# Kernel tuning notes

Hardware: AMD Instinct MI355X
Metric: run time of the kernel (lower is better)

The kernel has to match this reference:

```python
import jax, jax.numpy as jnp
import numpy as np

TSZ, BSZ, E, H = 1024, 8, 1024, 16


def setup_inputs() -> dict:
    key = jax.random.key(0)
    ks = jax.random.split(key, 7)
    s = 0.02
    return {
        "q": jax.random.normal(ks[0], (TSZ, BSZ, E), jnp.float32),
        "k": jax.random.normal(ks[1], (TSZ, BSZ, E), jnp.float32),
        "v": jax.random.normal(ks[2], (TSZ, BSZ, E), jnp.float32),
        "in_proj_weight": jax.random.normal(ks[3], (3 * E, E), jnp.float32) * s,
        "in_proj_bias": jax.random.normal(ks[4], (3 * E,), jnp.float32) * s,
        "out_proj_weight": jax.random.normal(ks[5], (E, E), jnp.float32) * s,
        "out_proj_bias": jax.random.normal(ks[6], (E,), jnp.float32) * s,
        "num_heads": H,
    }


def reference(q, k, v, in_proj_weight, in_proj_bias, out_proj_weight, out_proj_bias, num_heads):
    tsz, bsz, embed_dim = q.shape
    head_dim = embed_dim // num_heads
    scaling = float(head_dim) ** -0.5

    # in-projections (F.linear: x @ W.T + b), weight sliced into q/k/v chunks
    qp = q @ in_proj_weight[:embed_dim].T + in_proj_bias[:embed_dim]
    kp = k @ in_proj_weight[embed_dim:2 * embed_dim].T + in_proj_bias[embed_dim:2 * embed_dim]
    vp = v @ in_proj_weight[2 * embed_dim:].T + in_proj_bias[2 * embed_dim:]
    qp = qp * scaling

    # (tsz, bsz, E) -> (bsz*H, tsz, head_dim)
    def to_heads(x):
        return x.reshape(tsz, bsz * num_heads, head_dim).transpose(1, 0, 2)

    qh, kh, vh = to_heads(qp), to_heads(kp), to_heads(vp)

    # scaled dot-product attention (no mask, dropout p=0)
    scores = jnp.einsum('bqd,bkd->bqk', qh, kh)  # [bsz*H, tsz, tsz]
    weights = jax.nn.softmax(scores, axis=-1)
    attn = jnp.einsum('bqk,bkd->bqd', weights, vh)

    # back to (tsz, bsz, E), then out projection
    attn = attn.transpose(1, 0, 2).reshape(tsz, bsz, embed_dim)
    out = attn @ out_proj_weight.T + out_proj_bias
    return out
```

## Files before the change

kernel.cpp:

```cpp
#include <hip/hip_runtime.h>

typedef __bf16 bf16;
typedef __attribute__((ext_vector_type(8))) __bf16 v8bf;
typedef __attribute__((ext_vector_type(4))) __bf16 v4bf;
typedef __attribute__((ext_vector_type(4))) float f32x4;

static_assert(sizeof(v8bf) == 16, "v8bf must be 16B");

#define MFMA16(a, b, c) __builtin_amdgcn_mfma_f32_16x16x32_bf16((a), (b), (c), 0, 0, 0)

__device__ __forceinline__ void async_lds16(const bf16* g, bf16* l) {
  __builtin_amdgcn_global_load_lds(
      (__attribute__((address_space(1))) void*)(g),
      (__attribute__((address_space(3))) void*)(l), 16, 0, 0);
}

__global__ __launch_bounds__(256) void cvt_kernel(
    const float* __restrict__ q, const float* __restrict__ k,
    const float* __restrict__ v, const float* __restrict__ wi,
    const float* __restrict__ wo, bf16* __restrict__ xq, bf16* __restrict__ xk,
    bf16* __restrict__ xv, bf16* __restrict__ Wb, bf16* __restrict__ Wob) {
  int idx = blockIdx.x * 256 + threadIdx.x;
  const float4* src;
  v4bf* dst;
  int off;
  if (idx < 2097152)      { src = (const float4*)q;  dst = (v4bf*)xq;  off = idx; }
  else if (idx < 4194304) { src = (const float4*)k;  dst = (v4bf*)xk;  off = idx - 2097152; }
  else if (idx < 6291456) { src = (const float4*)v;  dst = (v4bf*)xv;  off = idx - 4194304; }
  else if (idx < 7077888) { src = (const float4*)wi; dst = (v4bf*)Wb;  off = idx - 6291456; }
  else                    { src = (const float4*)wo; dst = (v4bf*)Wob; off = idx - 7077888; }
  float4 f = src[off];
  v4bf b;
  b[0] = (bf16)f.x; b[1] = (bf16)f.y; b[2] = (bf16)f.z; b[3] = (bf16)f.w;
  dst[off] = b;
}

#define AB2_(AB) (((AB) + 2) % 3)

#define STG_A4(AB, KO)                                                        \
  do {                                                                        \
    _Pragma("unroll") for (int cc = 0; cc < 4; ++cc)                          \
        async_lds16(Xa + (size_t)cc * 65536 + srcoff + (KO),                  \
                    Asmb + (AB) * 8192 + cc * 2048 + wdst);                   \
  } while (0)

#define STG_B2(BB, KO)                                                        \
  do {                                                                        \
    _Pragma("unroll") for (int cc = 0; cc < 2; ++cc)                          \
        async_lds16(Wbase + (size_t)cc * 65536 + srcoff + (KO),               \
                    Bsmb + (BB) * 4096 + cc * 2048 + wdst);                   \
  } while (0)

#define RD_A(AB, G)                                                           \
  _Pragma("unroll") for (int f = 0; f < 4; ++f)                               \
      ar[f] = *(const v8bf*)&Asmb[(AB) * 8192 + arow + (G) * 2048 +           \
                                  f * 512 + slot8];

#define RD_B(BB)                                                              \
  _Pragma("unroll") for (int nf = 0; nf < 4; ++nf)                            \
      br[nf] = *(const v8bf*)&Bsmb[(BB) * 4096 + brow + nf * 512 + slot8];

#define MM(OFF)                                                               \
  __builtin_amdgcn_s_setprio(1);                                              \
  _Pragma("unroll") for (int f = 0; f < 4; ++f)                               \
      _Pragma("unroll") for (int nf = 0; nf < 4; ++nf)                        \
          acc[(OFF) + f][nf] = MFMA16(ar[f], br[nf], acc[(OFF) + f][nf]);     \
  __builtin_amdgcn_s_setprio(0);

#define STEP(T, AB, BB, SB, SA, VM)                                           \
  do {                                                                        \
    v8bf ar[4], br[4];                                                        \
    RD_A(AB, 0);                                                              \
    RD_B(BB);                                                                 \
    if (SB) STG_B2((BB) ^ 1, ((T) + 1) * 32);                                 \
    __builtin_amdgcn_s_barrier();                                             \
    MM(0);                                                                    \
    RD_A(AB, 1);                                                              \
    if (SA) STG_A4(AB2_(AB), ((T) + 2) * 32);                                 \
    if ((VM) == 4) { asm volatile("s_waitcnt vmcnt(4)" ::: "memory"); }       \
    else if ((VM) == 0) { asm volatile("s_waitcnt vmcnt(0)" ::: "memory"); }  \
    __builtin_amdgcn_s_barrier();                                             \
    MM(4);                                                                    \
  } while (0)

#define GEMM_PRELUDE()                                                        \
  const int tid = threadIdx.x;                                                \
  const int w = tid >> 6, l = tid & 63, quad = l >> 4, lr = l & 15;           \
  const int wmg = w >> 1, wng = w & 1;                                        \
  const int slot8 = (quad ^ ((lr >> 1) & 3)) * 8;                             \
  const int arow = (wmg * 128 + lr) * 32;                                     \
  const int brow = (wng * 64 + lr) * 32;                                      \
  const int wdst = (tid & ~63) * 8;                                           \
  const int srow = tid >> 2;                                                  \
  const int srcoff = srow * 1024 + (((tid & 3) ^ ((srow >> 1) & 3)) * 8);     \
  f32x4 acc[8][4] = {};                                                       \
  STG_A4(0, 0);                                                               \
  STG_B2(0, 0);                                                               \
  STG_A4(1, 32);                                                              \
  asm volatile("s_waitcnt vmcnt(4)" ::: "memory");                            \
  __builtin_amdgcn_s_barrier();                                               \
  _Pragma("unroll 1") for (int tt = 0; tt < 30; tt += 6) {                    \
    STEP(tt + 0, 0, 0, 1, 1, 4);                                              \
    STEP(tt + 1, 1, 1, 1, 1, 4);                                              \
    STEP(tt + 2, 2, 0, 1, 1, 4);                                              \
    STEP(tt + 3, 0, 1, 1, 1, 4);                                              \
    STEP(tt + 4, 1, 0, 1, 1, 4);                                              \
    STEP(tt + 5, 2, 1, 1, 1, 4);                                              \
  }                                                                           \
  STEP(30, 0, 0, 1, 0, 0);                                                    \
  STEP(31, 1, 1, 0, 0, -1);

__global__ __launch_bounds__(256, 2) void qkv_proj_kernel(
    const bf16* __restrict__ xq, const bf16* __restrict__ xk,
    const bf16* __restrict__ xv, const bf16* __restrict__ Wb,
    const float* __restrict__ bias, bf16* __restrict__ oq,
    bf16* __restrict__ ok, bf16* __restrict__ ov) {
  __shared__ bf16 Asm3[3][8192];
  __shared__ bf16 Bsm3[2][4096];
  bf16* Asmb = &Asm3[0][0];
  bf16* Bsmb = &Bsm3[0][0];
  const int L = blockIdx.x;
  const int g = L >> 5;
  const int c = g >> 3;
  const int n0 = (g & 7) * 128;
  const int m0 = (L & 31) * 256;
  const bf16* X = (c == 0) ? xq : (c == 1) ? xk : xv;
  bf16* outp = (c == 0) ? oq : (c == 1) ? ok : ov;
  const bf16* Xa = X + (size_t)m0 * 1024;
  const bf16* Wbase = Wb + ((size_t)(c * 1024 + n0)) * 1024;

  GEMM_PRELUDE();

  const float scale = (c == 0) ? 0.125f : 1.0f;
#pragma unroll
  for (int mf = 0; mf < 8; ++mf)
#pragma unroll
    for (int nf = 0; nf < 4; ++nf) {
      const int n = n0 + wng * 64 + nf * 16 + lr;
      const float bn = bias[c * 1024 + n];
      const int hh = n >> 6, d = n & 63;
#pragma unroll
      for (int j = 0; j < 4; ++j) {
        const int m = m0 + wmg * 128 + (mf >> 2) * 64 + (mf & 3) * 16 +
                      quad * 4 + j;
        const int t_ = m >> 3, b = m & 7;
        outp[((size_t)((b * 16 + hh) * 1024 + t_)) * 64 + d] =
            (bf16)((acc[mf][nf][j] + bn) * scale);
      }
    }
}

__global__ __launch_bounds__(256) void transpose_v_kernel(const bf16* __restrict__ vin,
                                                          bf16* __restrict__ vout) {
  __shared__ bf16 tile[64][72];
  const int bh = blockIdx.x;
  const int t0 = blockIdx.y * 64;
  const int tid = threadIdx.x;
  const int row = tid >> 2, cg = (tid & 3) * 16;
  const bf16* src = vin + ((size_t)bh * 1024 + t0 + row) * 64 + cg;
#pragma unroll
  for (int i = 0; i < 2; ++i) {
    v8bf x = *(const v8bf*)(src + i * 8);
#pragma unroll
    for (int jj = 0; jj < 8; ++jj) tile[row][cg + i * 8 + jj] = x[jj];
  }
  __syncthreads();
  const int d = tid >> 2, tg = (tid & 3) * 16;
  bf16* dst = vout + ((size_t)bh * 64 + d) * 1024 + t0 + tg;
  v8bf o0, o1;
#pragma unroll
  for (int i = 0; i < 8; ++i) o0[i] = tile[tg + i][d];
#pragma unroll
  for (int i = 0; i < 8; ++i) o1[i] = tile[tg + 8 + i][d];
  *(v8bf*)dst = o0;
  *(v8bf*)(dst + 8) = o1;
}

#define KSTR 72
#define VSTR 136

__global__ __launch_bounds__(256, 2) void attn_kernel(const bf16* __restrict__ qh,
                                                      const bf16* __restrict__ kh,
                                                      const bf16* __restrict__ vT,
                                                      bf16* __restrict__ attn_out) {
  __shared__ bf16 Ksm[128 * KSTR];
  __shared__ bf16 Vsm[64 * VSTR];
  __shared__ bf16 Psm[128 * VSTR];
  const int L = blockIdx.x;
  const int bh = (L & 7) * 16 + ((L >> 3) & 15);
  const int t0 = (L >> 7) * 128;
  const int tid = threadIdx.x;
  const int w = tid >> 6, l = tid & 63, quad = l >> 4, lr = l & 15;
  const int qr0 = t0 + w * 32;

  const bf16* khead = kh + (size_t)bh * 1024 * 64;
  const bf16* vhead = vT + (size_t)bh * 64 * 1024;

  const size_t qbase = ((size_t)bh * 1024 + qr0 + lr) * 64 + quad * 8;
  const v8bf bq00 = *(const v8bf*)(qh + qbase);
  const v8bf bq01 = *(const v8bf*)(qh + qbase + 32);
  const v8bf bq10 = *(const v8bf*)(qh + qbase + 1024);
  const v8bf bq11 = *(const v8bf*)(qh + qbase + 1024 + 32);

  const int krow = tid >> 1, kd = (tid & 1) * 32;
  const int vrow = tid >> 2, vk = (tid & 3) * 32;
  const bf16* kg = khead + (size_t)krow * 64 + kd;
  const bf16* vg = vhead + (size_t)vrow * 1024 + vk;
  bf16* Kw = &Ksm[krow * KSTR + kd];
  bf16* Vw = &Vsm[vrow * VSTR + vk];
  bf16* Pw = &Psm[w * 32 * VSTR];

  v8bf kst[4], vst[4];
#pragma unroll
  for (int i = 0; i < 4; ++i) kst[i] = *(const v8bf*)(kg + i * 8);
#pragma unroll
  for (int i = 0; i < 4; ++i) vst[i] = *(const v8bf*)(vg + i * 8);

  float rsum0 = 0.0f, rsum1 = 0.0f;
  f32x4 oacc0[4] = {}, oacc1[4] = {};

  for (int c = 0; c < 8; ++c) {
    __syncthreads();
#pragma unroll
    for (int i = 0; i < 4; ++i) *(v8bf*)(Kw + i * 8) = kst[i];
#pragma unroll
    for (int i = 0; i < 4; ++i) *(v8bf*)(Vw + i * 8) = vst[i];
    __syncthreads();
    if (c < 7) {
      const bf16* kg2 = kg + (size_t)(c + 1) * 128 * 64;
      const bf16* vg2 = vg + (c + 1) * 128;
#pragma unroll
      for (int i = 0; i < 4; ++i) kst[i] = *(const v8bf*)(kg2 + i * 8);
#pragma unroll
      for (int i = 0; i < 4; ++i) vst[i] = *(const v8bf*)(vg2 + i * 8);
    }

#pragma unroll
    for (int kt = 0; kt < 8; ++kt) {
      const v8bf ak0 = *(const v8bf*)&Ksm[(kt * 16 + lr) * KSTR + quad * 8];
      const v8bf ak1 = *(const v8bf*)&Ksm[(kt * 16 + lr) * KSTR + 32 + quad * 8];
      f32x4 a = {};
      a = MFMA16(ak0, bq00, a);
      a = MFMA16(ak1, bq01, a);
      f32x4 b = {};
      b = MFMA16(ak0, bq10, b);
      b = MFMA16(ak1, bq11, b);
      v4bf pb0, pb1;
#pragma unroll
      for (int j = 0; j < 4; ++j) {
        const float p0 = __expf(a[j]);
        const float p1 = __expf(b[j]);
        rsum0 += p0;
        rsum1 += p1;
        pb0[j] = (bf16)p0;
        pb1[j] = (bf16)p1;
      }
      *(v4bf*)(Pw + lr * VSTR + kt * 16 + quad * 4) = pb0;
      *(v4bf*)(Pw + (16 + lr) * VSTR + kt * 16 + quad * 4) = pb1;
    }

#pragma unroll
    for (int ks = 0; ks < 4; ++ks) {
      const v8bf pa0 = *(const v8bf*)(Pw + lr * VSTR + ks * 32 + quad * 8);
      const v8bf pa1 = *(const v8bf*)(Pw + (16 + lr) * VSTR + ks * 32 + quad * 8);
#pragma unroll
      for (int dt = 0; dt < 4; ++dt) {
        const v8bf vb = *(const v8bf*)&Vsm[(dt * 16 + lr) * VSTR + ks * 32 + quad * 8];
        oacc0[dt] = MFMA16(pa0, vb, oacc0[dt]);
        oacc1[dt] = MFMA16(pa1, vb, oacc1[dt]);
      }
    }
  }

  rsum0 += __shfl_xor(rsum0, 16);
  rsum0 += __shfl_xor(rsum0, 32);
  rsum1 += __shfl_xor(rsum1, 16);
  rsum1 += __shfl_xor(rsum1, 32);
  const float inv0 = 1.0f / rsum0;
  const float inv1 = 1.0f / rsum1;
  const int b = bh >> 4, h = bh & 15;
#pragma unroll
  for (int j = 0; j < 4; ++j) {
    const float i0 = __shfl(inv0, quad * 4 + j);
    const float i1 = __shfl(inv1, quad * 4 + j);
    const int t0j = qr0 + quad * 4 + j;
#pragma unroll
    for (int dt = 0; dt < 4; ++dt) {
      attn_out[((size_t)(t0j * 8 + b)) * 1024 + h * 64 + dt * 16 + lr] =
          (bf16)(oacc0[dt][j] * i0);
      attn_out[((size_t)((t0j + 16) * 8 + b)) * 1024 + h * 64 + dt * 16 + lr] =
          (bf16)(oacc1[dt][j] * i1);
    }
  }
}

__global__ __launch_bounds__(256, 2) void out_proj_kernel(const bf16* __restrict__ A,
                                                          const bf16* __restrict__ Wob,
                                                          const float* __restrict__ bias,
                                                          float* __restrict__ out) {
  __shared__ bf16 Asm3[3][8192];
  __shared__ bf16 Bsm3[2][4096];
  bf16* Asmb = &Asm3[0][0];
  bf16* Bsmb = &Bsm3[0][0];
  const int L = blockIdx.x;
  const int n0 = (L >> 5) * 128;
  const int m0 = (L & 31) * 256;
  const bf16* Xa = A + (size_t)m0 * 1024;
  const bf16* Wbase = Wob + (size_t)n0 * 1024;

  GEMM_PRELUDE();

#pragma unroll
  for (int mf = 0; mf < 8; ++mf)
#pragma unroll
    for (int nf = 0; nf < 4; ++nf) {
      const int n = n0 + wng * 64 + nf * 16 + lr;
      const float bn = bias[n];
#pragma unroll
      for (int j = 0; j < 4; ++j) {
        const int m = m0 + wmg * 128 + (mf >> 2) * 64 + (mf & 3) * 16 +
                      quad * 4 + j;
        out[(size_t)m * 1024 + n] = acc[mf][nf][j] + bn;
      }
    }
}

extern "C" void kernel_launch(void* const* d_in, const int* in_sizes, int n_in,
                              void* d_out, int out_size, void* d_ws, size_t ws_size,
                              hipStream_t stream) {
  const float* q  = (const float*)d_in[0];
  const float* k  = (const float*)d_in[1];
  const float* v  = (const float*)d_in[2];
  const float* wi = (const float*)d_in[3];
  const float* bi = (const float*)d_in[4];
  const float* wo = (const float*)d_in[5];
  const float* bo = (const float*)d_in[6];
  float* out = (float*)d_out;
  char* ws = (char*)d_ws;
  const size_t MB = (size_t)1 << 20;
  bf16* Wb     = (bf16*)(ws + 0 * MB);
  bf16* Wob    = (bf16*)(ws + 6 * MB);
  bf16* wsq    = (bf16*)(ws + 8 * MB);
  bf16* wsk    = (bf16*)(ws + 24 * MB);
  bf16* wsv    = (bf16*)(ws + 40 * MB);
  bf16* xv     = (bf16*)(ws + 56 * MB);
  bf16* wsvT   = (bf16*)(ws + 56 * MB);
  bf16* xq     = (bf16*)d_out;
  bf16* xk     = (bf16*)((char*)d_out + 16 * MB);
  bf16* wsattn = wsv;

  cvt_kernel<<<dim3(28672), dim3(256), 0, stream>>>(q, k, v, wi, wo, xq, xk, xv, Wb, Wob);
  qkv_proj_kernel<<<dim3(768), dim3(256), 0, stream>>>(xq, xk, xv, Wb, bi, wsq, wsk, wsv);
  transpose_v_kernel<<<dim3(128, 16), dim3(256), 0, stream>>>(wsv, wsvT);
  attn_kernel<<<dim3(1024), dim3(256), 0, stream>>>(wsq, wsk, wsvT, wsattn);
  out_proj_kernel<<<dim3(256), dim3(256), 0, stream>>>(wsattn, Wob, bo, out);
}
```

Measured before the change: 300.7 us.

## Switch GEMM pipeline from triple-buffered A to double-buffered A/B with higher occupancy

```diff
diff --git a/kernel.cpp b/kernel.cpp
--- a/kernel.cpp
+++ b/kernel.cpp
@@ -35,8 +35,6 @@
   dst[off] = b;
 }
 
-#define AB2_(AB) (((AB) + 2) % 3)
-
 #define STG_A4(AB, KO)                                                        \
   do {                                                                        \
     _Pragma("unroll") for (int cc = 0; cc < 4; ++cc)                          \
@@ -67,18 +65,19 @@
           acc[(OFF) + f][nf] = MFMA16(ar[f], br[nf], acc[(OFF) + f][nf]);     \
   __builtin_amdgcn_s_setprio(0);
 
-#define STEP(T, AB, BB, SB, SA, VM)                                           \
+#define STEP(T, AB, SG, VM)                                                   \
   do {                                                                        \
     v8bf ar[4], br[4];                                                        \
     RD_A(AB, 0);                                                              \
-    RD_B(BB);                                                                 \
-    if (SB) STG_B2((BB) ^ 1, ((T) + 1) * 32);                                 \
+    RD_B(AB);                                                                 \
+    if (SG) {                                                                 \
+      STG_A4((AB) ^ 1, ((T) + 1) * 32);                                       \
+      STG_B2((AB) ^ 1, ((T) + 1) * 32);                                       \
+    }                                                                         \
     __builtin_amdgcn_s_barrier();                                             \
     MM(0);                                                                    \
     RD_A(AB, 1);                                                              \
-    if (SA) STG_A4(AB2_(AB), ((T) + 2) * 32);                                 \
-    if ((VM) == 4) { asm volatile("s_waitcnt vmcnt(4)" ::: "memory"); }       \
-    else if ((VM) == 0) { asm volatile("s_waitcnt vmcnt(0)" ::: "memory"); }  \
+    if (VM) { asm volatile("s_waitcnt vmcnt(0)" ::: "memory"); }              \
     __builtin_amdgcn_s_barrier();                                             \
     MM(4);                                                                    \
   } while (0)
@@ -96,29 +95,24 @@
   f32x4 acc[8][4] = {};                                                       \
   STG_A4(0, 0);                                                               \
   STG_B2(0, 0);                                                               \
-  STG_A4(1, 32);                                                              \
-  asm volatile("s_waitcnt vmcnt(4)" ::: "memory");                            \
+  asm volatile("s_waitcnt vmcnt(0)" ::: "memory");                            \
   __builtin_amdgcn_s_barrier();                                               \
-  _Pragma("unroll 1") for (int tt = 0; tt < 30; tt += 6) {                    \
-    STEP(tt + 0, 0, 0, 1, 1, 4);                                              \
-    STEP(tt + 1, 1, 1, 1, 1, 4);                                              \
-    STEP(tt + 2, 2, 0, 1, 1, 4);                                              \
-    STEP(tt + 3, 0, 1, 1, 1, 4);                                              \
-    STEP(tt + 4, 1, 0, 1, 1, 4);                                              \
-    STEP(tt + 5, 2, 1, 1, 1, 4);                                              \
+  _Pragma("unroll 1") for (int tt = 0; tt < 30; tt += 2) {                    \
+    STEP(tt + 0, 0, 1, 1);                                                    \
+    STEP(tt + 1, 1, 1, 1);                                                    \
   }                                                                           \
-  STEP(30, 0, 0, 1, 0, 0);                                                    \
-  STEP(31, 1, 1, 0, 0, -1);
-
-__global__ __launch_bounds__(256, 2) void qkv_proj_kernel(
+  STEP(30, 0, 1, 1);                                                          \
+  STEP(31, 1, 0, 0);
+
+__global__ __launch_bounds__(256, 3) void qkv_proj_kernel(
     const bf16* __restrict__ xq, const bf16* __restrict__ xk,
     const bf16* __restrict__ xv, const bf16* __restrict__ Wb,
     const float* __restrict__ bias, bf16* __restrict__ oq,
     bf16* __restrict__ ok, bf16* __restrict__ ov) {
-  __shared__ bf16 Asm3[3][8192];
-  __shared__ bf16 Bsm3[2][4096];
-  bf16* Asmb = &Asm3[0][0];
-  bf16* Bsmb = &Bsm3[0][0];
+  __shared__ bf16 Asm2[2][8192];
+  __shared__ bf16 Bsm2[2][4096];
+  bf16* Asmb = &Asm2[0][0];
+  bf16* Bsmb = &Bsm2[0][0];
   const int L = blockIdx.x;
   const int g = L >> 5;
   const int c = g >> 3;
@@ -298,10 +292,10 @@
                                                           const bf16* __restrict__ Wob,
                                                           const float* __restrict__ bias,
                                                           float* __restrict__ out) {
-  __shared__ bf16 Asm3[3][8192];
-  __shared__ bf16 Bsm3[2][4096];
-  bf16* Asmb = &Asm3[0][0];
-  bf16* Bsmb = &Bsm3[0][0];
+  __shared__ bf16 Asm2[2][8192];
+  __shared__ bf16 Bsm2[2][4096];
+  bf16* Asmb = &Asm2[0][0];
+  bf16* Bsmb = &Bsm2[0][0];
   const int L = blockIdx.x;
   const int n0 = (L >> 5) * 128;
   const int m0 = (L & 31) * 256;
```

New measurement: 357.7 us. 1.19x slower.
